# Performance work log

Measured on AMD Instinct MI355X. Metric: run time of the kernel, lower is better.

## Reference

```python
import jax, jax.numpy as jnp
import numpy as np
import math

L, N, D = 1024, 64, 64
O = 1024

def setup_inputs() -> dict:
    key = jax.random.key(0)
    k1, k2 = jax.random.split(key)
    x = jax.random.normal(k1, (L, N, D), dtype=jnp.float32)
    upfold = jax.random.normal(k2, (O, N, D), dtype=jnp.float32)
    return {"x": x, "upfold": upfold}

def reference(x, upfold):
    # x: [L, N, D], upfold: [O, N, D]
    d = x.shape[-1]
    scale = 1.0 / math.sqrt(d)
    # affinities: [L, O, N]
    affinities = jnp.einsum('lnd,ond->lon', x, upfold) * scale
    # weighted sum with (sigmoid - 0.5) weights: [L, N, D]
    features = jnp.einsum('lon,ond->lnd', jax.nn.sigmoid(affinities) - 0.5, upfold)
    return features
```

## Files before the change

### kernel.cpp

```cpp
#include <hip/hip_runtime.h>
#include <stdint.h>

#define L_DIM 1024
#define N_DIM 64
#define D_DIM 64
#define O_DIM 1024
#define ND    4096
#define NT    16

typedef float    floatx16 __attribute__((ext_vector_type(16)));
typedef _Float16 half8    __attribute__((ext_vector_type(8)));
typedef _Float16 h2       __attribute__((ext_vector_type(2)));
typedef __fp16   fp16x2   __attribute__((ext_vector_type(2)));

#define BUF_STRIDE 17920

__device__ __forceinline__ uint32_t pkh2(float a, float b) {
    fp16x2 p = __builtin_amdgcn_cvt_pkrtz(a, b);
    return __builtin_bit_cast(uint32_t, p);
}

__device__ __forceinline__ half8 mk_frag(uint32_t a, uint32_t b, uint32_t c, uint32_t d) {
    union { uint32_t u[4]; half8 v; } U;
    U.u[0] = a; U.u[1] = b; U.u[2] = c; U.u[3] = d;
    return U.v;
}

__device__ __forceinline__ uint32_t psig(float s0, float s1) {
    const h2 HI = {(_Float16)41.6f,        (_Float16)41.6f};
    const h2 LO = {(_Float16)-41.6f,       (_Float16)-41.6f};
    const h2 SC = {(_Float16)0.0625f,      (_Float16)0.0625f};
    const h2 C0 = {(_Float16)0.03099238f,  (_Float16)0.03099238f};
    const h2 C1 = {(_Float16)-0.00842090f, (_Float16)-0.00842090f};
    const h2 C2 = {(_Float16)0.00151845f,  (_Float16)0.00151845f};
    const h2 C3 = {(_Float16)-1.02197e-4f, (_Float16)-1.02197e-4f};
    h2 s = __builtin_bit_cast(h2, pkh2(s0, s1));
    s = __builtin_elementwise_min(s, HI);
    s = __builtin_elementwise_max(s, LO);
    h2 ha = s * SC;
    h2 v  = ha * ha;
    h2 w  = C2 + v * C3;
    w     = C1 + v * w;
    w     = C0 + v * w;
    h2 f  = s * w;
    return __builtin_bit_cast(uint32_t, f);
}

__device__ __forceinline__ void load_tile(const float* ubase, int ot,
                                          int r8, int c, float4* va, float4* vb) {
    const float* pr = ubase + (size_t)(ot * 64 + 2 * r8) * ND + 4 * c;
    #pragma unroll
    for (int j = 0; j < 2; ++j) {
        va[j] = *(const float4*)(pr + (size_t)(32 * j) * ND);
        vb[j] = *(const float4*)(pr + (size_t)(32 * j) * ND + ND);
    }
}

__global__ void __launch_bounds__(256, 2)
corr_kernel(const float* __restrict__ x, const float* __restrict__ up,
            float* __restrict__ out)
{
    __shared__ __align__(16) unsigned char smem[2 * BUF_STRIDE];

    const int tid  = threadIdx.x;
    const int lane = tid & 63;
    const int wid  = tid >> 6;
    const int l31  = lane & 31;
    const int h    = lane >> 5;
    const int r8   = tid >> 4;
    const int c    = tid & 15;
    const int n    = blockIdx.x;
    const int lb   = blockIdx.y;
    const int lw   = lb * 128 + wid * 32 + l31;

    const float* ubase = up + (size_t)n * D_DIM;

    float4 va[2], vb[2];
    load_tile(ubase, 0, r8, c, va, vb);

    half8 Xf[4];
    {
        float (*Xs)[68] = (float (*)[68])smem;
        const int xr = tid >> 1;
        const int xh = tid & 1;
        const float* xsrc = x + (size_t)(lb * 128 + xr) * ND + n * D_DIM;
        #pragma unroll
        for (int j = 0; j < 8; ++j) {
            const int f4i = xh * 8 + j;
            *(float4*)&Xs[xr][4 * f4i] = *(const float4*)(xsrc + 4 * f4i);
        }
        __syncthreads();
        const int rl = wid * 32 + l31;
        #pragma unroll
        for (int kk = 0; kk < 4; ++kk) {
            float4 f1 = *(const float4*)&Xs[rl][16 * kk + 8 * h];
            float4 f2 = *(const float4*)&Xs[rl][16 * kk + 8 * h + 4];
            Xf[kk] = mk_frag(pkh2(f1.x, f1.y), pkh2(f1.z, f1.w),
                             pkh2(f2.x, f2.y), pkh2(f2.z, f2.w));
        }
        __syncthreads();
    }

    #pragma unroll
    for (int j = 0; j < 2; ++j) {
        uint16_t (*Ub)[72]  = (uint16_t (*)[72])(smem);
        uint32_t (*Ut2)[68] = (uint32_t (*)[68])(smem + 9216);
        *(uint2*)&Ub[2*r8 + 32*j][4*c] =
            make_uint2(pkh2(va[j].x, va[j].y), pkh2(va[j].z, va[j].w));
        *(uint2*)&Ub[2*r8 + 32*j + 1][4*c] =
            make_uint2(pkh2(vb[j].x, vb[j].y), pkh2(vb[j].z, vb[j].w));
        *(uint4*)&Ut2[r8 + 16*j][4*c] =
            make_uint4(pkh2(va[j].x, vb[j].x), pkh2(va[j].y, vb[j].y),
                       pkh2(va[j].z, vb[j].z), pkh2(va[j].w, vb[j].w));
    }
    load_tile(ubase, 1, r8, c, va, vb);
    __syncthreads();

    floatx16 F0, F1;
    #pragma unroll
    for (int i = 0; i < 16; ++i) { F0[i] = 0.0f; F1[i] = 0.0f; }

    for (int ot = 0; ot < NT; ++ot) {
        const int b = ot & 1;
        uint16_t (*Ub)[72]   = (uint16_t (*)[72])(smem + b * BUF_STRIDE);
        const uint32_t* utp  = (const uint32_t*)(smem + b * BUF_STRIDE + 9216);
        uint16_t (*Ubn)[72]  = (uint16_t (*)[72])(smem + (b ^ 1) * BUF_STRIDE);
        uint32_t (*Ut2n)[68] = (uint32_t (*)[68])(smem + (b ^ 1) * BUF_STRIDE + 9216);

        half8 A0k[4], A1k[4];
        #pragma unroll
        for (int kk = 0; kk < 4; ++kk) {
            A0k[kk] = *(const half8*)&Ub[l31][16 * kk + 8 * h];
            A1k[kk] = *(const half8*)&Ub[32 + l31][16 * kk + 8 * h];
        }

        if (ot + 1 < NT) {
            #pragma unroll
            for (int j = 0; j < 2; ++j) {
                *(uint2*)&Ubn[2*r8 + 32*j][4*c] =
                    make_uint2(pkh2(va[j].x, va[j].y), pkh2(va[j].z, va[j].w));
                *(uint2*)&Ubn[2*r8 + 32*j + 1][4*c] =
                    make_uint2(pkh2(vb[j].x, vb[j].y), pkh2(vb[j].z, vb[j].w));
                *(uint4*)&Ut2n[r8 + 16*j][4*c] =
                    make_uint4(pkh2(va[j].x, vb[j].x), pkh2(va[j].y, vb[j].y),
                               pkh2(va[j].z, vb[j].z), pkh2(va[j].w, vb[j].w));
            }
        }
        if (ot + 2 < NT)
            load_tile(ubase, ot + 2, r8, c, va, vb);

        floatx16 S0, S1;
        #pragma unroll
        for (int i = 0; i < 16; ++i) { S0[i] = 0.0f; S1[i] = 0.0f; }
        #pragma unroll
        for (int kk = 0; kk < 4; ++kk) {
            S0 = __builtin_amdgcn_mfma_f32_32x32x16_f16(A0k[kk], Xf[kk], S0, 0, 0, 0);
            S1 = __builtin_amdgcn_mfma_f32_32x32x16_f16(A1k[kk], Xf[kk], S1, 0, 0, 0);
        }

        uint32_t P[16];
        #pragma unroll
        for (int m = 0; m < 8; ++m) P[m]     = psig(S0[2*m], S0[2*m+1]);
        #pragma unroll
        for (int m = 0; m < 8; ++m) P[8 + m] = psig(S1[2*m], S1[2*m+1]);

        uint32_t R[8];
        #pragma unroll
        for (int c2 = 0; c2 < 4; ++c2) {
            const uint32_t* Q = P + (c2 >> 1) * 8;
            const int t4 = (c2 & 1) * 4;
            R[2*c2]   = __shfl_xor(h ? Q[t4]     : Q[t4 + 2], 32);
            R[2*c2+1] = __shfl_xor(h ? Q[t4 + 1] : Q[t4 + 3], 32);
        }
        #pragma unroll
        for (int c2 = 0; c2 < 4; ++c2) {
            const uint32_t* Q = P + (c2 >> 1) * 8;
            const int t4 = (c2 & 1) * 4;
            half8 B = h ? mk_frag(R[2*c2], R[2*c2+1], Q[t4 + 2], Q[t4 + 3])
                        : mk_frag(Q[t4], Q[t4 + 1], R[2*c2], R[2*c2+1]);
            const int opb = 8 * c2 + 4 * h;
            uint32_t a0[4], a1[4];
            #pragma unroll
            for (int k = 0; k < 4; ++k) {
                a0[k] = utp[(opb + k) * 68 + l31];
                a1[k] = utp[(opb + k) * 68 + 32 + l31];
            }
            half8 A0 = mk_frag(a0[0], a0[1], a0[2], a0[3]);
            half8 A1 = mk_frag(a1[0], a1[1], a1[2], a1[3]);
            F0 = __builtin_amdgcn_mfma_f32_32x32x16_f16(A0, B, F0, 0, 0, 0);
            F1 = __builtin_amdgcn_mfma_f32_32x32x16_f16(A1, B, F1, 0, 0, 0);
        }
        __syncthreads();
    }

    float* op = out + (size_t)lw * ND + n * D_DIM;
    #pragma unroll
    for (int q = 0; q < 4; ++q) {
        float4 a; a.x = F0[4*q]; a.y = F0[4*q+1]; a.z = F0[4*q+2]; a.w = F0[4*q+3];
        *(float4*)(op + 8*q + 4*h) = a;
        float4 bq; bq.x = F1[4*q]; bq.y = F1[4*q+1]; bq.z = F1[4*q+2]; bq.w = F1[4*q+3];
        *(float4*)(op + 32 + 8*q + 4*h) = bq;
    }
}

extern "C" void kernel_launch(void* const* d_in, const int* in_sizes, int n_in,
                              void* d_out, int out_size, void* d_ws, size_t ws_size,
                              hipStream_t stream)
{
    const float* x  = (const float*)d_in[0];
    const float* up = (const float*)d_in[1];
    float* out      = (float*)d_out;
    dim3 grid(N_DIM, L_DIM / 128);
    corr_kernel<<<grid, dim3(256), 0, stream>>>(x, up, out);
}
```

Before: 103.3 us.

## Split O-tile across warp pairs with 64-row L blocks and shared-memory reduction

Each block now covers 64 L rows instead of 128, and its four warps form a 2x2 grid over L rows and halves of the O tile. Each warp computes one 32x32 affinity block per tile instead of two. The two O-halves' partial outputs are then summed through shared memory before the store. This doubles the grid and raises the occupancy hint to 4 blocks per SM to get more parallelism and latency hiding. In exchange, each block re-reads the full upfold stream for half as many rows, which doubles upfold traffic and fp16 conversion work per output, and a final reduction step is added.

```diff
diff --git a/kernel.cpp b/kernel.cpp
--- a/kernel.cpp
+++ b/kernel.cpp
@@ -56,7 +56,7 @@
     }
 }
 
-__global__ void __launch_bounds__(256, 2)
+__global__ void __launch_bounds__(256, 4)
 corr_kernel(const float* __restrict__ x, const float* __restrict__ up,
             float* __restrict__ out)
 {
@@ -65,13 +65,15 @@
     const int tid  = threadIdx.x;
     const int lane = tid & 63;
     const int wid  = tid >> 6;
+    const int li   = wid & 1;
+    const int oi   = wid >> 1;
     const int l31  = lane & 31;
     const int h    = lane >> 5;
     const int r8   = tid >> 4;
     const int c    = tid & 15;
     const int n    = blockIdx.x;
     const int lb   = blockIdx.y;
-    const int lw   = lb * 128 + wid * 32 + l31;
+    const int lw   = lb * 64 + li * 32 + l31;
 
     const float* ubase = up + (size_t)n * D_DIM;
 
@@ -81,16 +83,16 @@
     half8 Xf[4];
     {
         float (*Xs)[68] = (float (*)[68])smem;
-        const int xr = tid >> 1;
-        const int xh = tid & 1;
-        const float* xsrc = x + (size_t)(lb * 128 + xr) * ND + n * D_DIM;
-        #pragma unroll
-        for (int j = 0; j < 8; ++j) {
-            const int f4i = xh * 8 + j;
+        const int xr = tid >> 2;
+        const int xq = tid & 3;
+        const float* xsrc = x + (size_t)(lb * 64 + xr) * ND + n * D_DIM;
+        #pragma unroll
+        for (int j = 0; j < 4; ++j) {
+            const int f4i = xq * 4 + j;
             *(float4*)&Xs[xr][4 * f4i] = *(const float4*)(xsrc + 4 * f4i);
         }
         __syncthreads();
-        const int rl = wid * 32 + l31;
+        const int rl = li * 32 + l31;
         #pragma unroll
         for (int kk = 0; kk < 4; ++kk) {
             float4 f1 = *(const float4*)&Xs[rl][16 * kk + 8 * h];
@@ -127,12 +129,10 @@
         uint16_t (*Ubn)[72]  = (uint16_t (*)[72])(smem + (b ^ 1) * BUF_STRIDE);
         uint32_t (*Ut2n)[68] = (uint32_t (*)[68])(smem + (b ^ 1) * BUF_STRIDE + 9216);
 
-        half8 A0k[4], A1k[4];
-        #pragma unroll
-        for (int kk = 0; kk < 4; ++kk) {
-            A0k[kk] = *(const half8*)&Ub[l31][16 * kk + 8 * h];
-            A1k[kk] = *(const half8*)&Ub[32 + l31][16 * kk + 8 * h];
-        }
+        half8 Ak[4];
+        #pragma unroll
+        for (int kk = 0; kk < 4; ++kk)
+            Ak[kk] = *(const half8*)&Ub[oi * 32 + l31][16 * kk + 8 * h];
 
         if (ot + 1 < NT) {
             #pragma unroll
@@ -149,36 +149,30 @@
         if (ot + 2 < NT)
             load_tile(ubase, ot + 2, r8, c, va, vb);
 
-        floatx16 S0, S1;
-        #pragma unroll
-        for (int i = 0; i < 16; ++i) { S0[i] = 0.0f; S1[i] = 0.0f; }
-        #pragma unroll
-        for (int kk = 0; kk < 4; ++kk) {
-            S0 = __builtin_amdgcn_mfma_f32_32x32x16_f16(A0k[kk], Xf[kk], S0, 0, 0, 0);
-            S1 = __builtin_amdgcn_mfma_f32_32x32x16_f16(A1k[kk], Xf[kk], S1, 0, 0, 0);
-        }
-
-        uint32_t P[16];
-        #pragma unroll
-        for (int m = 0; m < 8; ++m) P[m]     = psig(S0[2*m], S0[2*m+1]);
-        #pragma unroll
-        for (int m = 0; m < 8; ++m) P[8 + m] = psig(S1[2*m], S1[2*m+1]);
-
-        uint32_t R[8];
-        #pragma unroll
-        for (int c2 = 0; c2 < 4; ++c2) {
-            const uint32_t* Q = P + (c2 >> 1) * 8;
-            const int t4 = (c2 & 1) * 4;
-            R[2*c2]   = __shfl_xor(h ? Q[t4]     : Q[t4 + 2], 32);
-            R[2*c2+1] = __shfl_xor(h ? Q[t4 + 1] : Q[t4 + 3], 32);
-        }
-        #pragma unroll
-        for (int c2 = 0; c2 < 4; ++c2) {
-            const uint32_t* Q = P + (c2 >> 1) * 8;
-            const int t4 = (c2 & 1) * 4;
-            half8 B = h ? mk_frag(R[2*c2], R[2*c2+1], Q[t4 + 2], Q[t4 + 3])
-                        : mk_frag(Q[t4], Q[t4 + 1], R[2*c2], R[2*c2+1]);
-            const int opb = 8 * c2 + 4 * h;
+        floatx16 S;
+        #pragma unroll
+        for (int i = 0; i < 16; ++i) S[i] = 0.0f;
+        #pragma unroll
+        for (int kk = 0; kk < 4; ++kk)
+            S = __builtin_amdgcn_mfma_f32_32x32x16_f16(Ak[kk], Xf[kk], S, 0, 0, 0);
+
+        uint32_t P[8];
+        #pragma unroll
+        for (int m = 0; m < 8; ++m) P[m] = psig(S[2*m], S[2*m+1]);
+
+        uint32_t R[4];
+        #pragma unroll
+        for (int c2 = 0; c2 < 2; ++c2) {
+            const int t4 = c2 * 4;
+            R[2*c2]   = __shfl_xor(h ? P[t4]     : P[t4 + 2], 32);
+            R[2*c2+1] = __shfl_xor(h ? P[t4 + 1] : P[t4 + 3], 32);
+        }
+        #pragma unroll
+        for (int c2 = 0; c2 < 2; ++c2) {
+            const int t4 = c2 * 4;
+            half8 B = h ? mk_frag(R[2*c2], R[2*c2+1], P[t4 + 2], P[t4 + 3])
+                        : mk_frag(P[t4], P[t4 + 1], R[2*c2], R[2*c2+1]);
+            const int opb = oi * 16 + 8 * c2 + 4 * h;
             uint32_t a0[4], a1[4];
             #pragma unroll
             for (int k = 0; k < 4; ++k) {
@@ -193,13 +187,33 @@
         __syncthreads();
     }
 
-    float* op = out + (size_t)lw * ND + n * D_DIM;
-    #pragma unroll
-    for (int q = 0; q < 4; ++q) {
-        float4 a; a.x = F0[4*q]; a.y = F0[4*q+1]; a.z = F0[4*q+2]; a.w = F0[4*q+3];
-        *(float4*)(op + 8*q + 4*h) = a;
-        float4 bq; bq.x = F1[4*q]; bq.y = F1[4*q+1]; bq.z = F1[4*q+2]; bq.w = F1[4*q+3];
-        *(float4*)(op + 32 + 8*q + 4*h) = bq;
+    {
+        float (*Fs)[68] = (float (*)[68])smem;
+        const int row = li * 32 + l31;
+        if (oi == 1) {
+            #pragma unroll
+            for (int q = 0; q < 4; ++q) {
+                float4 a; a.x = F0[4*q]; a.y = F0[4*q+1]; a.z = F0[4*q+2]; a.w = F0[4*q+3];
+                *(float4*)&Fs[row][8*q + 4*h] = a;
+                float4 bq; bq.x = F1[4*q]; bq.y = F1[4*q+1]; bq.z = F1[4*q+2]; bq.w = F1[4*q+3];
+                *(float4*)&Fs[row][32 + 8*q + 4*h] = bq;
+            }
+        }
+        __syncthreads();
+        if (oi == 0) {
+            float* op = out + (size_t)lw * ND + n * D_DIM;
+            #pragma unroll
+            for (int q = 0; q < 4; ++q) {
+                float4 t0 = *(const float4*)&Fs[row][8*q + 4*h];
+                float4 a; a.x = F0[4*q]   + t0.x; a.y = F0[4*q+1] + t0.y;
+                          a.z = F0[4*q+2] + t0.z; a.w = F0[4*q+3] + t0.w;
+                *(float4*)(op + 8*q + 4*h) = a;
+                float4 t1 = *(const float4*)&Fs[row][32 + 8*q + 4*h];
+                float4 bq; bq.x = F1[4*q]   + t1.x; bq.y = F1[4*q+1] + t1.y;
+                           bq.z = F1[4*q+2] + t1.z; bq.w = F1[4*q+3] + t1.w;
+                *(float4*)(op + 32 + 8*q + 4*h) = bq;
+            }
+        }
     }
 }
 
@@ -210,6 +224,6 @@
     const float* x  = (const float*)d_in[0];
     const float* up = (const float*)d_in[1];
     float* out      = (float*)d_out;
-    dim3 grid(N_DIM, L_DIM / 128);
+    dim3 grid(N_DIM, L_DIM / 64);
     corr_kernel<<<grid, dim3(256), 0, stream>>>(x, up, out);
 }
```

Measured after the change: 103.3 us. About the same (-0.0%).

## Double block size and stage four O-tiles per barrier span

Applied to the files above, without the earlier changes.

Each block now covers 256 L rows with 512 threads, so each upfold tile loaded and converted to fp16 serves twice as many rows. O-tiles are staged four at a time in double-buffered spans, with the two thread halves splitting the loading, which cuts barriers from 16 to 4 per block. Warps start at staggered tiles so the packing and LDS reads spread out. The transposed U image gets a padded layout that allows 64-bit LDS reads. The costs are much more shared memory per block, fewer blocks in the grid, and possibly lower occupancy.

```diff
diff --git a/kernel.cpp b/kernel.cpp
--- a/kernel.cpp
+++ b/kernel.cpp
@@ -6,14 +6,19 @@
 #define D_DIM 64
 #define O_DIM 1024
 #define ND    4096
-#define NT    16
+
+#define UB_BYTES  9216
+#define UTT_BYTES 9728
+#define IMG_BYTES (UB_BYTES + UTT_BYTES)
+#define SPAN      4
+#define NSPAN     4
+#define BUF_BYTES (SPAN * IMG_BYTES)
+#define SMEM_BYTES (2 * BUF_BYTES)
 
 typedef float    floatx16 __attribute__((ext_vector_type(16)));
 typedef _Float16 half8    __attribute__((ext_vector_type(8)));
 typedef _Float16 h2       __attribute__((ext_vector_type(2)));
 typedef __fp16   fp16x2   __attribute__((ext_vector_type(2)));
-
-#define BUF_STRIDE 17920
 
 __device__ __forceinline__ uint32_t pkh2(float a, float b) {
     fp16x2 p = __builtin_amdgcn_cvt_pkrtz(a, b);
@@ -56,34 +61,52 @@
     }
 }
 
-__global__ void __launch_bounds__(256, 2)
+__device__ __forceinline__ void pack_tile(unsigned char* tb, int r8, int c,
+                                          const float4* va, const float4* vb) {
+    uint16_t (*Ub)[72]  = (uint16_t (*)[72])tb;
+    uint32_t (*UtT)[38] = (uint32_t (*)[38])(tb + UB_BYTES);
+    #pragma unroll
+    for (int j = 0; j < 2; ++j) {
+        *(uint2*)&Ub[2*r8 + 32*j][4*c] =
+            make_uint2(pkh2(va[j].x, va[j].y), pkh2(va[j].z, va[j].w));
+        *(uint2*)&Ub[2*r8 + 32*j + 1][4*c] =
+            make_uint2(pkh2(vb[j].x, vb[j].y), pkh2(vb[j].z, vb[j].w));
+        const int op = r8 + 16*j;
+        UtT[4*c + 0][op] = pkh2(va[j].x, vb[j].x);
+        UtT[4*c + 1][op] = pkh2(va[j].y, vb[j].y);
+        UtT[4*c + 2][op] = pkh2(va[j].z, vb[j].z);
+        UtT[4*c + 3][op] = pkh2(va[j].w, vb[j].w);
+    }
+}
+
+__global__ void __launch_bounds__(512, 2)
 corr_kernel(const float* __restrict__ x, const float* __restrict__ up,
             float* __restrict__ out)
 {
-    __shared__ __align__(16) unsigned char smem[2 * BUF_STRIDE];
+    __shared__ __align__(16) unsigned char smem[SMEM_BYTES];
 
     const int tid  = threadIdx.x;
     const int lane = tid & 63;
     const int wid  = tid >> 6;
     const int l31  = lane & 31;
     const int h    = lane >> 5;
-    const int r8   = tid >> 4;
-    const int c    = tid & 15;
+    const int sid  = tid >> 8;
+    const int ttid = tid & 255;
+    const int r8   = ttid >> 4;
+    const int c    = ttid & 15;
     const int n    = blockIdx.x;
     const int lb   = blockIdx.y;
-    const int lw   = lb * 128 + wid * 32 + l31;
+    const int lw   = lb * 256 + wid * 32 + l31;
+    const int stoff = (((wid >> 2) * 2) + (wid & 3)) & 3;
 
     const float* ubase = up + (size_t)n * D_DIM;
-
-    float4 va[2], vb[2];
-    load_tile(ubase, 0, r8, c, va, vb);
 
     half8 Xf[4];
     {
         float (*Xs)[68] = (float (*)[68])smem;
         const int xr = tid >> 1;
         const int xh = tid & 1;
-        const float* xsrc = x + (size_t)(lb * 128 + xr) * ND + n * D_DIM;
+        const float* xsrc = x + (size_t)(lb * 256 + xr) * ND + n * D_DIM;
         #pragma unroll
         for (int j = 0; j < 8; ++j) {
             const int f4i = xh * 8 + j;
@@ -101,94 +124,94 @@
         __syncthreads();
     }
 
-    #pragma unroll
-    for (int j = 0; j < 2; ++j) {
-        uint16_t (*Ub)[72]  = (uint16_t (*)[72])(smem);
-        uint32_t (*Ut2)[68] = (uint32_t (*)[68])(smem + 9216);
-        *(uint2*)&Ub[2*r8 + 32*j][4*c] =
-            make_uint2(pkh2(va[j].x, va[j].y), pkh2(va[j].z, va[j].w));
-        *(uint2*)&Ub[2*r8 + 32*j + 1][4*c] =
-            make_uint2(pkh2(vb[j].x, vb[j].y), pkh2(vb[j].z, vb[j].w));
-        *(uint4*)&Ut2[r8 + 16*j][4*c] =
-            make_uint4(pkh2(va[j].x, vb[j].x), pkh2(va[j].y, vb[j].y),
-                       pkh2(va[j].z, vb[j].z), pkh2(va[j].w, vb[j].w));
-    }
-    load_tile(ubase, 1, r8, c, va, vb);
+    float4 va[2][2], vb[2][2];
+    #pragma unroll
+    for (int k = 0; k < 2; ++k)
+        load_tile(ubase, 2*sid + k, r8, c, va[k], vb[k]);
+    #pragma unroll
+    for (int k = 0; k < 2; ++k)
+        pack_tile(smem + (size_t)(2*sid + k) * IMG_BYTES, r8, c, va[k], vb[k]);
+    #pragma unroll
+    for (int k = 0; k < 2; ++k)
+        load_tile(ubase, SPAN + 2*sid + k, r8, c, va[k], vb[k]);
     __syncthreads();
 
     floatx16 F0, F1;
     #pragma unroll
     for (int i = 0; i < 16; ++i) { F0[i] = 0.0f; F1[i] = 0.0f; }
 
-    for (int ot = 0; ot < NT; ++ot) {
-        const int b = ot & 1;
-        uint16_t (*Ub)[72]   = (uint16_t (*)[72])(smem + b * BUF_STRIDE);
-        const uint32_t* utp  = (const uint32_t*)(smem + b * BUF_STRIDE + 9216);
-        uint16_t (*Ubn)[72]  = (uint16_t (*)[72])(smem + (b ^ 1) * BUF_STRIDE);
-        uint32_t (*Ut2n)[68] = (uint32_t (*)[68])(smem + (b ^ 1) * BUF_STRIDE + 9216);
-
-        half8 A0k[4], A1k[4];
+    for (int s = 0; s < NSPAN; ++s) {
+        const unsigned char* bufc = smem + (size_t)(s & 1) * BUF_BYTES;
+        unsigned char*       bufn = smem + (size_t)((s & 1) ^ 1) * BUF_BYTES;
+
         #pragma unroll
-        for (int kk = 0; kk < 4; ++kk) {
-            A0k[kk] = *(const half8*)&Ub[l31][16 * kk + 8 * h];
-            A1k[kk] = *(const half8*)&Ub[32 + l31][16 * kk + 8 * h];
-        }
-
-        if (ot + 1 < NT) {
-            #pragma unroll
-            for (int j = 0; j < 2; ++j) {
-                *(uint2*)&Ubn[2*r8 + 32*j][4*c] =
-                    make_uint2(pkh2(va[j].x, va[j].y), pkh2(va[j].z, va[j].w));
-                *(uint2*)&Ubn[2*r8 + 32*j + 1][4*c] =
-                    make_uint2(pkh2(vb[j].x, vb[j].y), pkh2(vb[j].z, vb[j].w));
-                *(uint4*)&Ut2n[r8 + 16*j][4*c] =
-                    make_uint4(pkh2(va[j].x, vb[j].x), pkh2(va[j].y, vb[j].y),
-                               pkh2(va[j].z, vb[j].z), pkh2(va[j].w, vb[j].w));
-            }
-        }
-        if (ot + 2 < NT)
-            load_tile(ubase, ot + 2, r8, c, va, vb);
-
-        floatx16 S0, S1;
-        #pragma unroll
-        for (int i = 0; i < 16; ++i) { S0[i] = 0.0f; S1[i] = 0.0f; }
-        #pragma unroll
-        for (int kk = 0; kk < 4; ++kk) {
-            S0 = __builtin_amdgcn_mfma_f32_32x32x16_f16(A0k[kk], Xf[kk], S0, 0, 0, 0);
-            S1 = __builtin_amdgcn_mfma_f32_32x32x16_f16(A1k[kk], Xf[kk], S1, 0, 0, 0);
-        }
-
-        uint32_t P[16];
-        #pragma unroll
-        for (int m = 0; m < 8; ++m) P[m]     = psig(S0[2*m], S0[2*m+1]);
-        #pragma unroll
-        for (int m = 0; m < 8; ++m) P[8 + m] = psig(S1[2*m], S1[2*m+1]);
-
-        uint32_t R[8];
-        #pragma unroll
-        for (int c2 = 0; c2 < 4; ++c2) {
-            const uint32_t* Q = P + (c2 >> 1) * 8;
-            const int t4 = (c2 & 1) * 4;
-            R[2*c2]   = __shfl_xor(h ? Q[t4]     : Q[t4 + 2], 32);
-            R[2*c2+1] = __shfl_xor(h ? Q[t4 + 1] : Q[t4 + 3], 32);
-        }
-        #pragma unroll
-        for (int c2 = 0; c2 < 4; ++c2) {
-            const uint32_t* Q = P + (c2 >> 1) * 8;
-            const int t4 = (c2 & 1) * 4;
-            half8 B = h ? mk_frag(R[2*c2], R[2*c2+1], Q[t4 + 2], Q[t4 + 3])
-                        : mk_frag(Q[t4], Q[t4 + 1], R[2*c2], R[2*c2+1]);
-            const int opb = 8 * c2 + 4 * h;
-            uint32_t a0[4], a1[4];
-            #pragma unroll
-            for (int k = 0; k < 4; ++k) {
-                a0[k] = utp[(opb + k) * 68 + l31];
-                a1[k] = utp[(opb + k) * 68 + 32 + l31];
-            }
-            half8 A0 = mk_frag(a0[0], a0[1], a0[2], a0[3]);
-            half8 A1 = mk_frag(a1[0], a1[1], a1[2], a1[3]);
-            F0 = __builtin_amdgcn_mfma_f32_32x32x16_f16(A0, B, F0, 0, 0, 0);
-            F1 = __builtin_amdgcn_mfma_f32_32x32x16_f16(A1, B, F1, 0, 0, 0);
+        for (int i = 0; i < SPAN; ++i) {
+            if (s + 1 < NSPAN) {
+                #pragma unroll
+                for (int k = 0; k < 2; ++k) {
+                    if (i == 2*k + (wid & 1)) {
+                        pack_tile(bufn + (size_t)(2*sid + k) * IMG_BYTES,
+                                  r8, c, va[k], vb[k]);
+                        if (s + 2 < NSPAN)
+                            load_tile(ubase, (s + 2) * SPAN + 2*sid + k,
+                                      r8, c, va[k], vb[k]);
+                    }
+                }
+            }
+
+            const int ti = (stoff + i) & 3;
+            const unsigned char* tb = bufc + (size_t)ti * IMG_BYTES;
+            const uint16_t (*Ub)[72] = (const uint16_t (*)[72])tb;
+            const uint32_t* utT      = (const uint32_t*)(tb + UB_BYTES);
+
+            half8 A0k[4], A1k[4];
+            #pragma unroll
+            for (int kk = 0; kk < 4; ++kk) {
+                A0k[kk] = *(const half8*)&Ub[l31][16 * kk + 8 * h];
+                A1k[kk] = *(const half8*)&Ub[32 + l31][16 * kk + 8 * h];
+            }
+
+            floatx16 S0, S1;
+            #pragma unroll
+            for (int i2 = 0; i2 < 16; ++i2) { S0[i2] = 0.0f; S1[i2] = 0.0f; }
+            #pragma unroll
+            for (int kk = 0; kk < 4; ++kk) {
+                S0 = __builtin_amdgcn_mfma_f32_32x32x16_f16(A0k[kk], Xf[kk], S0, 0, 0, 0);
+                S1 = __builtin_amdgcn_mfma_f32_32x32x16_f16(A1k[kk], Xf[kk], S1, 0, 0, 0);
+            }
+
+            uint32_t P[16];
+            #pragma unroll
+            for (int m = 0; m < 8; ++m) P[m]     = psig(S0[2*m], S0[2*m+1]);
+            #pragma unroll
+            for (int m = 0; m < 8; ++m) P[8 + m] = psig(S1[2*m], S1[2*m+1]);
+
+            uint32_t R[8];
+            #pragma unroll
+            for (int c2 = 0; c2 < 4; ++c2) {
+                const uint32_t* Q = P + (c2 >> 1) * 8;
+                const int t4 = (c2 & 1) * 4;
+                R[2*c2]   = __shfl_xor(h ? Q[t4]     : Q[t4 + 2], 32);
+                R[2*c2+1] = __shfl_xor(h ? Q[t4 + 1] : Q[t4 + 3], 32);
+            }
+            #pragma unroll
+            for (int c2 = 0; c2 < 4; ++c2) {
+                const uint32_t* Q = P + (c2 >> 1) * 8;
+                const int t4 = (c2 & 1) * 4;
+                half8 B = h ? mk_frag(R[2*c2], R[2*c2+1], Q[t4 + 2], Q[t4 + 3])
+                            : mk_frag(Q[t4], Q[t4 + 1], R[2*c2], R[2*c2+1]);
+                const int opb = 8 * c2 + 4 * h;
+                const uint32_t* r0 = utT + l31 * 38;
+                const uint32_t* r1 = utT + (32 + l31) * 38;
+                uint2 q0 = *(const uint2*)(r0 + opb);
+                uint2 q1 = *(const uint2*)(r0 + opb + 2);
+                uint2 q2 = *(const uint2*)(r1 + opb);
+                uint2 q3 = *(const uint2*)(r1 + opb + 2);
+                half8 A0 = mk_frag(q0.x, q0.y, q1.x, q1.y);
+                half8 A1 = mk_frag(q2.x, q2.y, q3.x, q3.y);
+                F0 = __builtin_amdgcn_mfma_f32_32x32x16_f16(A0, B, F0, 0, 0, 0);
+                F1 = __builtin_amdgcn_mfma_f32_32x32x16_f16(A1, B, F1, 0, 0, 0);
+            }
         }
         __syncthreads();
     }
@@ -210,6 +233,6 @@
     const float* x  = (const float*)d_in[0];
     const float* up = (const float*)d_in[1];
     float* out      = (float*)d_out;
-    dim3 grid(N_DIM, L_DIM / 128);
-    corr_kernel<<<grid, dim3(256), 0, stream>>>(x, up, out);
-}
+    dim3 grid(N_DIM, L_DIM / 256);
+    corr_kernel<<<grid, dim3(512), 0, stream>>>(x, up, out);
+}
```

New measurement: 101.9 us. Within noise of the previous version (-1.4%).

## Restructure into two-team split-O blocks with fragment-ordered LDS tiles and reduction

Applied to the files above, without the earlier changes.

Each block now covers 256 L rows with 512 threads in two teams of four waves. Each team handles half of every 64-wide O tile (32 rows) and the two partial sums are combined through LDS at the end. The upfold tiles are packed straight into MFMA fragment order in LDS, eight tiles per phase, so fragment loads become contiguous 16-byte reads, and register double-buffering of fragments replaces the per-tile global prefetch. This aims to improve reuse of upfold across more L rows and to cut LDS bank conflicts and per-tile syncs. In exchange it uses a large 128KB LDS image, exposes global load latency in bulk phases, and halves the grid to 256 blocks.

```diff
diff --git a/kernel.cpp b/kernel.cpp
--- a/kernel.cpp
+++ b/kernel.cpp
@@ -6,14 +6,15 @@
 #define D_DIM 64
 #define O_DIM 1024
 #define ND    4096
-#define NT    16
+
+#define TILE_BYTES 16384
+#define HALF_TILES 8
+#define IMG_LDS   (HALF_TILES * TILE_BYTES)
 
 typedef float    floatx16 __attribute__((ext_vector_type(16)));
 typedef _Float16 half8    __attribute__((ext_vector_type(8)));
 typedef _Float16 h2       __attribute__((ext_vector_type(2)));
 typedef __fp16   fp16x2   __attribute__((ext_vector_type(2)));
-
-#define BUF_STRIDE 17920
 
 __device__ __forceinline__ uint32_t pkh2(float a, float b) {
     fp16x2 p = __builtin_amdgcn_cvt_pkrtz(a, b);
@@ -46,160 +47,192 @@
     return __builtin_bit_cast(uint32_t, f);
 }
 
-__device__ __forceinline__ void load_tile(const float* ubase, int ot,
-                                          int r8, int c, float4* va, float4* vb) {
-    const float* pr = ubase + (size_t)(ot * 64 + 2 * r8) * ND + 4 * c;
-    #pragma unroll
-    for (int j = 0; j < 2; ++j) {
-        va[j] = *(const float4*)(pr + (size_t)(32 * j) * ND);
-        vb[j] = *(const float4*)(pr + (size_t)(32 * j) * ND + ND);
-    }
-}
-
-__global__ void __launch_bounds__(256, 2)
-corr_kernel(const float* __restrict__ x, const float* __restrict__ up,
-            float* __restrict__ out)
-{
-    __shared__ __align__(16) unsigned char smem[2 * BUF_STRIDE];
+__device__ __forceinline__ void pack_chunks(const float* up_n, int ot, int w, int lane,
+                                            unsigned char* tb)
+{
+    {
+        const int t  = w >> 2, kk = w & 3;
+        const int ot_row = ot * 64 + t * 32 + (lane & 31);
+        const int d0 = 16 * kk + 8 * (lane >> 5);
+        const float* src = up_n + (size_t)ot_row * ND + d0;
+        float4 f1 = *(const float4*)src;
+        float4 f2 = *(const float4*)(src + 4);
+        *(uint4*)(tb + t * 4096 + kk * 1024 + lane * 16) =
+            make_uint4(pkh2(f1.x, f1.y), pkh2(f1.z, f1.w),
+                       pkh2(f2.x, f2.y), pkh2(f2.z, f2.w));
+    }
+    {
+        const int t  = w >> 2, c2 = (w >> 1) & 1, r = w & 1;
+        const int d   = r * 32 + (lane & 31);
+        const int opb = t * 16 + 8 * c2 + 4 * (lane >> 5);
+        const float* sp = up_n + (size_t)(ot * 64 + 2 * opb) * ND + d;
+        uint32_t u0 = pkh2(sp[0],                 sp[(size_t)ND]);
+        uint32_t u1 = pkh2(sp[(size_t)2 * ND],    sp[(size_t)3 * ND]);
+        uint32_t u2 = pkh2(sp[(size_t)4 * ND],    sp[(size_t)5 * ND]);
+        uint32_t u3 = pkh2(sp[(size_t)6 * ND],    sp[(size_t)7 * ND]);
+        *(uint4*)(tb + 8192 + t * 4096 + c2 * 2048 + r * 1024 + lane * 16) =
+            make_uint4(u0, u1, u2, u3);
+    }
+}
+
+__device__ __forceinline__ void load_frags(const unsigned char* tb, int team, int lane,
+                                           half8* Ak, half8* G2) {
+    const unsigned char* g1 = tb + team * 4096 + (size_t)lane * 16;
+    #pragma unroll
+    for (int kk = 0; kk < 4; ++kk)
+        Ak[kk] = *(const half8*)(g1 + kk * 1024);
+    const unsigned char* g2 = tb + 8192 + team * 4096 + (size_t)lane * 16;
+    #pragma unroll
+    for (int i = 0; i < 4; ++i)
+        G2[i] = *(const half8*)(g2 + i * 1024);
+}
+
+__device__ __forceinline__ void compute_tile(const half8* Ak, const half8* G2,
+                                             const half8* Xf0, const half8* Xf1, int h,
+                                             floatx16& F00, floatx16& F01,
+                                             floatx16& F10, floatx16& F11)
+{
+    floatx16 S0, S1;
+    #pragma unroll
+    for (int i = 0; i < 16; ++i) { S0[i] = 0.0f; S1[i] = 0.0f; }
+    #pragma unroll
+    for (int kk = 0; kk < 4; ++kk) {
+        S0 = __builtin_amdgcn_mfma_f32_32x32x16_f16(Ak[kk], Xf0[kk], S0, 0, 0, 0);
+        S1 = __builtin_amdgcn_mfma_f32_32x32x16_f16(Ak[kk], Xf1[kk], S1, 0, 0, 0);
+    }
+
+    uint32_t P0[8], P1[8];
+    #pragma unroll
+    for (int m = 0; m < 8; ++m) { P0[m] = psig(S0[2*m], S0[2*m+1]);
+                                  P1[m] = psig(S1[2*m], S1[2*m+1]); }
+
+    uint32_t R0[4], R1[4];
+    #pragma unroll
+    for (int c2 = 0; c2 < 2; ++c2) {
+        const int t4 = c2 * 4;
+        R0[2*c2]   = __shfl_xor(h ? P0[t4]     : P0[t4 + 2], 32);
+        R0[2*c2+1] = __shfl_xor(h ? P0[t4 + 1] : P0[t4 + 3], 32);
+        R1[2*c2]   = __shfl_xor(h ? P1[t4]     : P1[t4 + 2], 32);
+        R1[2*c2+1] = __shfl_xor(h ? P1[t4 + 1] : P1[t4 + 3], 32);
+    }
+    #pragma unroll
+    for (int c2 = 0; c2 < 2; ++c2) {
+        const int t4 = c2 * 4;
+        half8 B0 = h ? mk_frag(R0[2*c2], R0[2*c2+1], P0[t4 + 2], P0[t4 + 3])
+                     : mk_frag(P0[t4], P0[t4 + 1], R0[2*c2], R0[2*c2+1]);
+        half8 B1 = h ? mk_frag(R1[2*c2], R1[2*c2+1], P1[t4 + 2], P1[t4 + 3])
+                     : mk_frag(P1[t4], P1[t4 + 1], R1[2*c2], R1[2*c2+1]);
+        F00 = __builtin_amdgcn_mfma_f32_32x32x16_f16(G2[2*c2],     B0, F00, 0, 0, 0);
+        F01 = __builtin_amdgcn_mfma_f32_32x32x16_f16(G2[2*c2 + 1], B0, F01, 0, 0, 0);
+        F10 = __builtin_amdgcn_mfma_f32_32x32x16_f16(G2[2*c2],     B1, F10, 0, 0, 0);
+        F11 = __builtin_amdgcn_mfma_f32_32x32x16_f16(G2[2*c2 + 1], B1, F11, 0, 0, 0);
+    }
+}
+
+__global__ void __launch_bounds__(512, 2)
+corr_lds(const float* __restrict__ x, const float* __restrict__ up,
+         float* __restrict__ out)
+{
+    __shared__ __align__(16) unsigned char simg[IMG_LDS];
+    float (*Xs)[68] = (float (*)[68])simg;
 
     const int tid  = threadIdx.x;
     const int lane = tid & 63;
     const int wid  = tid >> 6;
+    const int team = wid >> 2;
+    const int tw   = wid & 3;
     const int l31  = lane & 31;
     const int h    = lane >> 5;
-    const int r8   = tid >> 4;
-    const int c    = tid & 15;
     const int n    = blockIdx.x;
     const int lb   = blockIdx.y;
-    const int lw   = lb * 128 + wid * 32 + l31;
-
-    const float* ubase = up + (size_t)n * D_DIM;
-
-    float4 va[2], vb[2];
-    load_tile(ubase, 0, r8, c, va, vb);
-
-    half8 Xf[4];
+
+    const float* up_n = up + (size_t)n * D_DIM;
+
+    half8 Xf0[4], Xf1[4];
     {
-        float (*Xs)[68] = (float (*)[68])smem;
         const int xr = tid >> 1;
         const int xh = tid & 1;
-        const float* xsrc = x + (size_t)(lb * 128 + xr) * ND + n * D_DIM;
+        const float* xsrc = x + (size_t)(lb * 256 + xr) * ND + n * D_DIM;
         #pragma unroll
         for (int j = 0; j < 8; ++j) {
             const int f4i = xh * 8 + j;
             *(float4*)&Xs[xr][4 * f4i] = *(const float4*)(xsrc + 4 * f4i);
         }
         __syncthreads();
-        const int rl = wid * 32 + l31;
+        const int rl0 = tw * 64 + l31;
+        const int rl1 = rl0 + 32;
         #pragma unroll
         for (int kk = 0; kk < 4; ++kk) {
-            float4 f1 = *(const float4*)&Xs[rl][16 * kk + 8 * h];
-            float4 f2 = *(const float4*)&Xs[rl][16 * kk + 8 * h + 4];
-            Xf[kk] = mk_frag(pkh2(f1.x, f1.y), pkh2(f1.z, f1.w),
-                             pkh2(f2.x, f2.y), pkh2(f2.z, f2.w));
-        }
-        __syncthreads();
-    }
-
-    #pragma unroll
-    for (int j = 0; j < 2; ++j) {
-        uint16_t (*Ub)[72]  = (uint16_t (*)[72])(smem);
-        uint32_t (*Ut2)[68] = (uint32_t (*)[68])(smem + 9216);
-        *(uint2*)&Ub[2*r8 + 32*j][4*c] =
-            make_uint2(pkh2(va[j].x, va[j].y), pkh2(va[j].z, va[j].w));
-        *(uint2*)&Ub[2*r8 + 32*j + 1][4*c] =
-            make_uint2(pkh2(vb[j].x, vb[j].y), pkh2(vb[j].z, vb[j].w));
-        *(uint4*)&Ut2[r8 + 16*j][4*c] =
-            make_uint4(pkh2(va[j].x, vb[j].x), pkh2(va[j].y, vb[j].y),
-                       pkh2(va[j].z, vb[j].z), pkh2(va[j].w, vb[j].w));
-    }
-    load_tile(ubase, 1, r8, c, va, vb);
+            float4 f1 = *(const float4*)&Xs[rl0][16 * kk + 8 * h];
+            float4 f2 = *(const float4*)&Xs[rl0][16 * kk + 8 * h + 4];
+            Xf0[kk] = mk_frag(pkh2(f1.x, f1.y), pkh2(f1.z, f1.w),
+                              pkh2(f2.x, f2.y), pkh2(f2.z, f2.w));
+            float4 f3 = *(const float4*)&Xs[rl1][16 * kk + 8 * h];
+            float4 f4v = *(const float4*)&Xs[rl1][16 * kk + 8 * h + 4];
+            Xf1[kk] = mk_frag(pkh2(f3.x, f3.y), pkh2(f3.z, f3.w),
+                              pkh2(f4v.x, f4v.y), pkh2(f4v.z, f4v.w));
+        }
+        __syncthreads();
+    }
+
+    floatx16 F00, F01, F10, F11;
+    #pragma unroll
+    for (int i = 0; i < 16; ++i) { F00[i] = 0.0f; F01[i] = 0.0f;
+                                   F10[i] = 0.0f; F11[i] = 0.0f; }
+
+    for (int hb = 0; hb < 2; ++hb) {
+        for (int tt = 0; tt < HALF_TILES; ++tt)
+            pack_chunks(up_n, hb * HALF_TILES + tt, wid, lane,
+                        simg + (size_t)tt * TILE_BYTES);
+        __syncthreads();
+
+        half8 AkE[4], G2E[4], AkO[4], G2O[4];
+        load_frags(simg, team, lane, AkE, G2E);
+        for (int t2 = 0; t2 < HALF_TILES; t2 += 2) {
+            load_frags(simg + (size_t)(t2 + 1) * TILE_BYTES, team, lane, AkO, G2O);
+            compute_tile(AkE, G2E, Xf0, Xf1, h, F00, F01, F10, F11);
+            if (t2 + 2 < HALF_TILES)
+                load_frags(simg + (size_t)(t2 + 2) * TILE_BYTES, team, lane, AkE, G2E);
+            compute_tile(AkO, G2O, Xf0, Xf1, h, F00, F01, F10, F11);
+        }
+        __syncthreads();
+    }
+
+    if (team == 1) {
+        #pragma unroll
+        for (int lh = 0; lh < 2; ++lh) {
+            const int row = tw * 64 + lh * 32 + l31;
+            const floatx16& A = lh ? F10 : F00;
+            const floatx16& Bq = lh ? F11 : F01;
+            #pragma unroll
+            for (int q = 0; q < 4; ++q) {
+                float4 a; a.x = A[4*q]; a.y = A[4*q+1]; a.z = A[4*q+2]; a.w = A[4*q+3];
+                *(float4*)&Xs[row][8*q + 4*h] = a;
+                float4 b2; b2.x = Bq[4*q]; b2.y = Bq[4*q+1]; b2.z = Bq[4*q+2]; b2.w = Bq[4*q+3];
+                *(float4*)&Xs[row][32 + 8*q + 4*h] = b2;
+            }
+        }
+    }
     __syncthreads();
-
-    floatx16 F0, F1;
-    #pragma unroll
-    for (int i = 0; i < 16; ++i) { F0[i] = 0.0f; F1[i] = 0.0f; }
-
-    for (int ot = 0; ot < NT; ++ot) {
-        const int b = ot & 1;
-        uint16_t (*Ub)[72]   = (uint16_t (*)[72])(smem + b * BUF_STRIDE);
-        const uint32_t* utp  = (const uint32_t*)(smem + b * BUF_STRIDE + 9216);
-        uint16_t (*Ubn)[72]  = (uint16_t (*)[72])(smem + (b ^ 1) * BUF_STRIDE);
-        uint32_t (*Ut2n)[68] = (uint32_t (*)[68])(smem + (b ^ 1) * BUF_STRIDE + 9216);
-
-        half8 A0k[4], A1k[4];
-        #pragma unroll
-        for (int kk = 0; kk < 4; ++kk) {
-            A0k[kk] = *(const half8*)&Ub[l31][16 * kk + 8 * h];
-            A1k[kk] = *(const half8*)&Ub[32 + l31][16 * kk + 8 * h];
-        }
-
-        if (ot + 1 < NT) {
+    if (team == 0) {
+        #pragma unroll
+        for (int lh = 0; lh < 2; ++lh) {
+            const int row = tw * 64 + lh * 32 + l31;
+            const floatx16& A = lh ? F10 : F00;
+            const floatx16& Bq = lh ? F11 : F01;
+            float* op = out + (size_t)(lb * 256 + row) * ND + n * D_DIM;
             #pragma unroll
-            for (int j = 0; j < 2; ++j) {
-                *(uint2*)&Ubn[2*r8 + 32*j][4*c] =
-                    make_uint2(pkh2(va[j].x, va[j].y), pkh2(va[j].z, va[j].w));
-                *(uint2*)&Ubn[2*r8 + 32*j + 1][4*c] =
-                    make_uint2(pkh2(vb[j].x, vb[j].y), pkh2(vb[j].z, vb[j].w));
-                *(uint4*)&Ut2n[r8 + 16*j][4*c] =
-                    make_uint4(pkh2(va[j].x, vb[j].x), pkh2(va[j].y, vb[j].y),
-                               pkh2(va[j].z, vb[j].z), pkh2(va[j].w, vb[j].w));
+            for (int q = 0; q < 4; ++q) {
+                float4 t0 = *(const float4*)&Xs[row][8*q + 4*h];
+                float4 a; a.x = A[4*q]   + t0.x; a.y = A[4*q+1] + t0.y;
+                          a.z = A[4*q+2] + t0.z; a.w = A[4*q+3] + t0.w;
+                *(float4*)(op + 8*q + 4*h) = a;
+                float4 t1 = *(const float4*)&Xs[row][32 + 8*q + 4*h];
+                float4 b2; b2.x = Bq[4*q]   + t1.x; b2.y = Bq[4*q+1] + t1.y;
+                           b2.z = Bq[4*q+2] + t1.z; b2.w = Bq[4*q+3] + t1.w;
+                *(float4*)(op + 32 + 8*q + 4*h) = b2;
             }
         }
-        if (ot + 2 < NT)
-            load_tile(ubase, ot + 2, r8, c, va, vb);
-
-        floatx16 S0, S1;
-        #pragma unroll
-        for (int i = 0; i < 16; ++i) { S0[i] = 0.0f; S1[i] = 0.0f; }
-        #pragma unroll
-        for (int kk = 0; kk < 4; ++kk) {
-            S0 = __builtin_amdgcn_mfma_f32_32x32x16_f16(A0k[kk], Xf[kk], S0, 0, 0, 0);
-            S1 = __builtin_amdgcn_mfma_f32_32x32x16_f16(A1k[kk], Xf[kk], S1, 0, 0, 0);
-        }
-
-        uint32_t P[16];
-        #pragma unroll
-        for (int m = 0; m < 8; ++m) P[m]     = psig(S0[2*m], S0[2*m+1]);
-        #pragma unroll
-        for (int m = 0; m < 8; ++m) P[8 + m] = psig(S1[2*m], S1[2*m+1]);
-
-        uint32_t R[8];
-        #pragma unroll
-        for (int c2 = 0; c2 < 4; ++c2) {
-            const uint32_t* Q = P + (c2 >> 1) * 8;
-            const int t4 = (c2 & 1) * 4;
-            R[2*c2]   = __shfl_xor(h ? Q[t4]     : Q[t4 + 2], 32);
-            R[2*c2+1] = __shfl_xor(h ? Q[t4 + 1] : Q[t4 + 3], 32);
-        }
-        #pragma unroll
-        for (int c2 = 0; c2 < 4; ++c2) {
-            const uint32_t* Q = P + (c2 >> 1) * 8;
-            const int t4 = (c2 & 1) * 4;
-            half8 B = h ? mk_frag(R[2*c2], R[2*c2+1], Q[t4 + 2], Q[t4 + 3])
-                        : mk_frag(Q[t4], Q[t4 + 1], R[2*c2], R[2*c2+1]);
-            const int opb = 8 * c2 + 4 * h;
-            uint32_t a0[4], a1[4];
-            #pragma unroll
-            for (int k = 0; k < 4; ++k) {
-                a0[k] = utp[(opb + k) * 68 + l31];
-                a1[k] = utp[(opb + k) * 68 + 32 + l31];
-            }
-            half8 A0 = mk_frag(a0[0], a0[1], a0[2], a0[3]);
-            half8 A1 = mk_frag(a1[0], a1[1], a1[2], a1[3]);
-            F0 = __builtin_amdgcn_mfma_f32_32x32x16_f16(A0, B, F0, 0, 0, 0);
-            F1 = __builtin_amdgcn_mfma_f32_32x32x16_f16(A1, B, F1, 0, 0, 0);
-        }
-        __syncthreads();
-    }
-
-    float* op = out + (size_t)lw * ND + n * D_DIM;
-    #pragma unroll
-    for (int q = 0; q < 4; ++q) {
-        float4 a; a.x = F0[4*q]; a.y = F0[4*q+1]; a.z = F0[4*q+2]; a.w = F0[4*q+3];
-        *(float4*)(op + 8*q + 4*h) = a;
-        float4 bq; bq.x = F1[4*q]; bq.y = F1[4*q+1]; bq.z = F1[4*q+2]; bq.w = F1[4*q+3];
-        *(float4*)(op + 32 + 8*q + 4*h) = bq;
     }
 }
 
@@ -210,6 +243,6 @@
     const float* x  = (const float*)d_in[0];
     const float* up = (const float*)d_in[1];
     float* out      = (float*)d_out;
-    dim3 grid(N_DIM, L_DIM / 128);
-    corr_kernel<<<grid, dim3(256), 0, stream>>>(x, up, out);
-}
+    dim3 grid(N_DIM, L_DIM / 256);
+    corr_lds<<<grid, dim3(512), 0, stream>>>(x, up, out);
+}
```

New measurement: 112.5 us. 1.09x slower.
